# Performance work log

Measured on AMD Instinct MI355X. Metric: run time of the kernel, lower is better.

Reference implementation:

```python
import jax, jax.numpy as jnp
import numpy as np

MODES, WIDTH, DEPTH, IN_F, OUT_F, HID = 8, 16, 3, 1, 1, 64


def setup_inputs() -> dict:
    key = jax.random.key(0)
    ks = jax.random.split(key, 12)
    B, H, W = 8, 512, 512
    scale = 1.0 / (WIDTH * WIDTH)
    inp = {
        'x': jax.random.normal(ks[0], (B, IN_F, H, W), dtype=jnp.float32),
        'fc0_w': jax.random.normal(ks[1], (IN_F, WIDTH), dtype=jnp.float32) * 0.5,
        'fc0_b': jax.random.normal(ks[2], (WIDTH,), dtype=jnp.float32) * 0.1,
        # complex spectral weights stored as real/imag parts, stacked over depth
        'spec_wr': jax.random.normal(ks[3], (DEPTH, WIDTH, WIDTH, MODES, MODES), dtype=jnp.float32) * scale,
        'spec_wi': jax.random.normal(ks[4], (DEPTH, WIDTH, WIDTH, MODES, MODES), dtype=jnp.float32) * scale,
        # 1x1 convs as [depth, out, in] matmuls + bias
        'conv_w': jax.random.normal(ks[5], (DEPTH, WIDTH, WIDTH), dtype=jnp.float32) * 0.25,
        'conv_b': jax.random.normal(ks[6], (DEPTH, WIDTH), dtype=jnp.float32) * 0.1,
        'fc1_w': jax.random.normal(ks[7], (WIDTH, HID), dtype=jnp.float32) * 0.25,
        'fc1_b': jax.random.normal(ks[8], (HID,), dtype=jnp.float32) * 0.1,
        'fc2_w': jax.random.normal(ks[9], (HID, OUT_F), dtype=jnp.float32) * 0.125,
        'fc2_b': jax.random.normal(ks[10], (OUT_F,), dtype=jnp.float32) * 0.1,
    }
    return inp


def _spectral_conv(x, w):
    # x: [B, Ci, H, W] real; w: [Ci, Co, m, m] complex
    B, C, H, W = x.shape
    m = w.shape[2]
    x_ft = jnp.fft.rfft2(x, norm='forward')  # [B, Ci, H, W//2+1]
    out_modes = jnp.einsum('bixy,ioxy->boxy', x_ft[:, :, :m, :m], w)
    out_ft = jnp.zeros((B, w.shape[1], H, W // 2 + 1), dtype=out_modes.dtype)
    out_ft = out_ft.at[:, :, :m, :m].set(out_modes)
    return jnp.fft.irfft2(out_ft, s=(H, W), norm='forward')


def reference(x, fc0_w, fc0_b, spec_wr, spec_wi, conv_w, conv_b, fc1_w, fc1_b, fc2_w, fc2_b):
    # lift: [B,C,H,W] -> channels-last linear -> [B,width,H,W]
    h = jnp.einsum('bchw,cd->bdhw', x, fc0_w) + fc0_b[None, :, None, None]
    for d in range(DEPTH):
        w_c = (spec_wr[d] + 1j * spec_wi[d]).astype(jnp.complex64)
        y = _spectral_conv(h, w_c)
        local = jnp.einsum('bchw,oc->bohw', h, conv_w[d]) + conv_b[d][None, :, None, None]
        h = y + local
    h = jnp.einsum('bchw,cd->bdhw', h, fc1_w) + fc1_b[None, :, None, None]
    h = jax.nn.relu(h)
    out = jnp.einsum('bchw,cd->bdhw', h, fc2_w) + fc2_b[None, :, None, None]
    return out
```

## Files before the change

### kernel.cpp

```cpp
#include <hip/hip_runtime.h>
#include <math.h>

#define NB 8
#define NH 512
#define NW 512
#define ANG512 0.01227184630308513f
#define SPEC_D 16384

__device__ __forceinline__ void treduce16(float* p, float* tb, float* dst, int tid) {
    #pragma unroll
    for (int j = 0; j < 16; ++j) p[j] += __shfl_xor(p[j], 1);
    if (!(tid & 1)) {
        const int s = tid >> 1;
        #pragma unroll
        for (int j = 0; j < 16; ++j) tb[s * 17 + j] = p[j];
    }
    __syncthreads();
    {
        const int q = tid >> 4, g = tid & 15;
        float v = 0.f;
        #pragma unroll
        for (int j = 0; j < 8; ++j) v += tb[(g + 16 * j) * 17 + q];
        #pragma unroll
        for (int m = 1; m < 16; m <<= 1) v += __shfl_xor(v, m, 16);
        if (g == 0) dst[q] = v;
    }
    __syncthreads();
}

__global__ __launch_bounds__(256) void k_rowdft(const float* __restrict__ x,
                                                float* __restrict__ R) {
    __shared__ float tb[128 * 17];
    __shared__ float red[16];
    const int tid = threadIdx.x;
    const int b = blockIdx.x >> 9;
    const int row = blockIdx.x & 511;
    const float* xr = x + ((size_t)(b * NH + row)) * NW;
    const float xa = xr[tid], xb = xr[tid + 256];
    const float a = xa + xb, d = xa - xb;

    float p[16];
    float c1, s1;
    __sincosf(ANG512 * (float)tid, &s1, &c1);
    p[0] = a;      p[8] = 0.f;
    p[1] = d * c1; p[9] = -d * s1;
    {
        const float c2k = 2.f * c1;
        float ckm = 1.f, skm = 0.f, ck = c1, sk = s1;
        #pragma unroll
        for (int k = 2; k < 8; ++k) {
            const float cn = fmaf(c2k, ck, -ckm);
            const float sn = fmaf(c2k, sk, -skm);
            ckm = ck; skm = sk; ck = cn; sk = sn;
            const float v = (k & 1) ? d : a;
            p[k] = v * ck;
            p[8 + k] = -v * sk;
        }
    }
    treduce16(p, tb, red, tid);
    if (tid < 16) R[((size_t)(b * NH + row)) * 16 + tid] = red[tid];
}

__global__ __launch_bounds__(256) void k_modes(
        const float* __restrict__ R,
        const float* __restrict__ spec_wr, const float* __restrict__ spec_wi,
        const float* __restrict__ conv_w, const float* __restrict__ conv_b,
        const float* __restrict__ fc0_w, const float* __restrict__ fc0_b,
        const float* __restrict__ fc1_w, const float* __restrict__ fc1_b,
        float* __restrict__ AH, float* __restrict__ gvec, float* __restrict__ Kvec) {
    __shared__ float Wr_s[3][16][16][8];
    __shared__ float Wi_s[3][16][16][8];
    __shared__ float tb[128 * 17];
    __shared__ float X2[16];
    __shared__ float Xr[16][8], Xi[16][8];
    __shared__ float Fr[16][8], Fi[16][8];
    __shared__ float Ar[16][8], Ai[16][8];
    __shared__ float Pm[2][256];
    __shared__ float fc1_s[1024];
    __shared__ float ps[64];

    const int tid = threadIdx.x;
    const int bb = blockIdx.x >> 3;
    const int kx = blockIdx.x & 7;

    {
        const int i = tid >> 4, o = tid & 15;
        #pragma unroll
        for (int d = 0; d < 3; ++d) {
            const size_t base = (size_t)d * SPEC_D + ((size_t)(i * 16 + o) * 64 + kx * 8);
            const float4* pr = (const float4*)(spec_wr + base);
            const float4* pi = (const float4*)(spec_wi + base);
            *(float4*)(&Wr_s[d][i][o][0]) = pr[0];
            *(float4*)(&Wr_s[d][i][o][4]) = pr[1];
            *(float4*)(&Wi_s[d][i][o][0]) = pi[0];
            *(float4*)(&Wi_s[d][i][o][4]) = pi[1];
        }
    }
    {
        const int o = tid >> 4, c = tid & 15;
        float s = 0.f;
        for (int k = 0; k < 16; ++k)
            s += conv_w[512 + o * 16 + k] * conv_w[256 + k * 16 + c];
        Pm[0][tid] = s;
    }
    Pm[1][tid] = conv_w[512 + tid];
    #pragma unroll
    for (int k = 0; k < 4; ++k) fc1_s[tid + k * 256] = fc1_w[tid + k * 256];

    float p[16];
    #pragma unroll
    for (int j = 0; j < 16; ++j) p[j] = 0.f;
    #pragma unroll
    for (int r2 = 0; r2 < 2; ++r2) {
        const int row = tid + r2 * 256;
        const float4* rp4 = (const float4*)(R + ((size_t)(bb * NH + row)) * 16);
        const float4 q0 = rp4[0], q1 = rp4[1], q2 = rp4[2], q3 = rp4[3];
        const float re[8] = {q0.x, q0.y, q0.z, q0.w, q1.x, q1.y, q1.z, q1.w};
        const float im[8] = {q2.x, q2.y, q2.z, q2.w, q3.x, q3.y, q3.z, q3.w};
        const int m = (kx * row) & 511;
        float cm, sm;
        __sincosf(ANG512 * (float)m, &sm, &cm);
        #pragma unroll
        for (int k = 0; k < 8; ++k) {
            p[k]     += re[k] * cm + im[k] * sm;
            p[8 + k] += im[k] * cm - re[k] * sm;
        }
    }
    treduce16(p, tb, X2, tid);

    const bool act = (tid < 128);
    const int o = tid >> 3, ky = tid & 7;
    if (act) {
        const float inv = 1.f / (512.f * 512.f);
        float xr0 = fc0_w[o] * X2[ky] * inv;
        float xi0 = fc0_w[o] * X2[8 + ky] * inv;
        if (kx == 0 && ky == 0) xr0 += fc0_b[o];
        Xr[o][ky] = xr0; Xi[o][ky] = xi0;
        Ar[o][ky] = 0.f; Ai[o][ky] = 0.f;
    }
    __syncthreads();

    for (int dd = 0; dd < 3; ++dd) {
        if (act) {
            float fr = 0.f, fi = 0.f;
            #pragma unroll
            for (int i = 0; i < 16; ++i) {
                const float wre = Wr_s[dd][i][o][ky];
                const float wim = Wi_s[dd][i][o][ky];
                const float xr0 = Xr[i][ky], xi0 = Xi[i][ky];
                fr += xr0 * wre - xi0 * wim;
                fi += xr0 * wim + xi0 * wre;
            }
            Fr[o][ky] = fr; Fi[o][ky] = fi;
        }
        __syncthreads();
        float xnr = 0.f, xni = 0.f;
        if (act) {
            float ar, ai;
            if (dd == 2) {
                ar = Fr[o][ky]; ai = Fi[o][ky];
            } else {
                ar = 0.f; ai = 0.f;
                #pragma unroll
                for (int c = 0; c < 16; ++c) {
                    const float pv = Pm[dd][o * 16 + c];
                    ar = fmaf(pv, Fr[c][ky], ar);
                    ai = fmaf(pv, Fi[c][ky], ai);
                }
            }
            Ar[o][ky] += ar; Ai[o][ky] += ai;
            if (dd < 2) {
                const float fr0 = Fr[o][ky], fi0 = Fi[o][ky];
                if (ky == 0) {
                    if (kx == 0) { xnr = fr0; xni = 0.f; }
                    else         { xnr = 0.5f * fr0; xni = 0.5f * fi0; }
                } else { xnr = fr0; xni = fi0; }
                #pragma unroll
                for (int c = 0; c < 16; ++c) {
                    const float cc = conv_w[dd * 256 + o * 16 + c];
                    xnr = fmaf(cc, Xr[c][ky], xnr);
                    xni = fmaf(cc, Xi[c][ky], xni);
                }
                if (kx == 0 && ky == 0) xnr += conv_b[dd * 16 + o];
            }
        }
        __syncthreads();
        if (act && dd < 2) { Xr[o][ky] = xnr; Xi[o][ky] = xni; }
        __syncthreads();
    }

    #pragma unroll
    for (int k2 = 0; k2 < 2; ++k2) {
        const int idx = tid + k2 * 256;
        const int hd = idx >> 3, ky2 = idx & 7;
        float ar = 0.f, ai = 0.f;
        #pragma unroll
        for (int c = 0; c < 16; ++c) {
            const float f = fc1_s[c * 64 + hd];
            ar = fmaf(f, Ar[c][ky2], ar);
            ai = fmaf(f, Ai[c][ky2], ai);
        }
        const float ck = (ky2 == 0) ? 1.f : 2.f;
        const size_t off = ((((size_t)(bb * 64 + hd)) * 8 + ky2) * 8 + kx) * 2;
        AH[off] = ck * ar;
        AH[off + 1] = ck * ai;
    }

    if (blockIdx.x == 0) {
        if (tid < 16) {
            float su = 0.f, sb = 0.f;
            for (int c = 0; c < 16; ++c) {
                su += conv_w[tid * 16 + c] * fc0_w[c];
                sb += conv_w[tid * 16 + c] * fc0_b[c];
            }
            ps[tid] = su; ps[16 + tid] = sb;
        }
        __syncthreads();
        if (tid < 16) {
            float dv = 0.f, ev = conv_b[32 + tid];
            for (int k = 0; k < 16; ++k) {
                dv += Pm[0][tid * 16 + k] * ps[k];
                ev += Pm[0][tid * 16 + k] * (ps[16 + k] + conv_b[k]);
                ev += conv_w[512 + tid * 16 + k] * conv_b[16 + k];
            }
            ps[32 + tid] = dv; ps[48 + tid] = ev;
        }
        __syncthreads();
        if (tid < 64) {
            float g = 0.f, K = fc1_b[tid];
            for (int c = 0; c < 16; ++c) {
                g = fmaf(fc1_w[c * 64 + tid], ps[32 + c], g);
                K = fmaf(fc1_w[c * 64 + tid], ps[48 + c], K);
            }
            gvec[tid] = g; Kvec[tid] = K;
        }
    }
}

__global__ __launch_bounds__(256, 2) void k_head(
        const float* __restrict__ x, const float* __restrict__ AH,
        const float* __restrict__ gvec, const float* __restrict__ Kvec,
        const float* __restrict__ fc2_w, const float* __restrict__ fc2_b,
        float* __restrict__ out) {
    __shared__ float WHr[4][512];
    __shared__ float WHi[4][512];

    const int tid = threadIdx.x;
    const int b = blockIdx.x >> 7;
    const int rp = blockIdx.x & 127;
    const int rl = tid >> 6;
    const int row = rp * 4 + rl;
    const int w0 = tid & 63;

    const float* xp = x + ((size_t)(b * NH + row)) * NW + w0;
    float xv[8];
    #pragma unroll
    for (int j = 0; j < 8; ++j) xv[j] = xp[j * 64];

    {
        float c1, s1;
        __sincosf(ANG512 * (float)row, &s1, &c1);
        float ctr[8], str[8];
        ctr[0] = 1.f; str[0] = 0.f; ctr[1] = c1; str[1] = s1;
        const float c2k = 2.f * c1;
        #pragma unroll
        for (int k = 2; k < 8; ++k) {
            ctr[k] = fmaf(c2k, ctr[k - 1], -ctr[k - 2]);
            str[k] = fmaf(c2k, str[k - 1], -str[k - 2]);
        }
        #pragma unroll
        for (int j = 0; j < 8; ++j) {
            const int idx = w0 + j * 64;
            const int hd = idx >> 3, ky = idx & 7;
            const float4* ap = (const float4*)(AH + ((size_t)(b * 64 + hd) * 8 + ky) * 16);
            const float4 a0 = ap[0], a1 = ap[1], a2 = ap[2], a3 = ap[3];
            float wr = a0.x, wi = a0.y;
            wr = fmaf(a0.z, ctr[1], wr); wr = fmaf(-a0.w, str[1], wr);
            wi = fmaf(a0.z, str[1], wi); wi = fmaf(a0.w, ctr[1], wi);
            wr = fmaf(a1.x, ctr[2], wr); wr = fmaf(-a1.y, str[2], wr);
            wi = fmaf(a1.x, str[2], wi); wi = fmaf(a1.y, ctr[2], wi);
            wr = fmaf(a1.z, ctr[3], wr); wr = fmaf(-a1.w, str[3], wr);
            wi = fmaf(a1.z, str[3], wi); wi = fmaf(a1.w, ctr[3], wi);
            wr = fmaf(a2.x, ctr[4], wr); wr = fmaf(-a2.y, str[4], wr);
            wi = fmaf(a2.x, str[4], wi); wi = fmaf(a2.y, ctr[4], wi);
            wr = fmaf(a2.z, ctr[5], wr); wr = fmaf(-a2.w, str[5], wr);
            wi = fmaf(a2.z, str[5], wi); wi = fmaf(a2.w, ctr[5], wi);
            wr = fmaf(a3.x, ctr[6], wr); wr = fmaf(-a3.y, str[6], wr);
            wi = fmaf(a3.x, str[6], wi); wi = fmaf(a3.y, ctr[6], wi);
            wr = fmaf(a3.z, ctr[7], wr); wr = fmaf(-a3.w, str[7], wr);
            wi = fmaf(a3.z, str[7], wi); wi = fmaf(a3.w, ctr[7], wi);
            if (ky == 0) wr += Kvec[hd];
            WHr[rl][idx] = wr;
            WHi[rl][idx] = wi;
        }
    }
    __syncthreads();

    {
        float c1, s1;
        __sincosf(ANG512 * (float)w0, &s1, &c1);
        float ct[8], st[8];
        ct[0] = 1.f; st[0] = 0.f; ct[1] = c1; st[1] = s1;
        const float c2k = 2.f * c1;
        #pragma unroll
        for (int k = 2; k < 8; ++k) {
            ct[k] = fmaf(c2k, ct[k - 1], -ct[k - 2]);
            st[k] = fmaf(c2k, st[k - 1], -st[k - 2]);
        }
        const float r2c = 0.70710678118654752f;
        const float* WR = &WHr[rl][0];
        const float* WI = &WHi[rl][0];
        const float fc2b = fc2_b[0];
        float acc[8];
        #pragma unroll
        for (int j = 0; j < 8; ++j) acc[j] = fc2b;

        #pragma unroll 4
        for (int hd = 0; hd < 64; ++hd) {
            const float4* r4 = (const float4*)(WR + hd * 8);
            const float4 wa = r4[0], wb = r4[1];
            const float4* i4 = (const float4*)(WI + hd * 8);
            const float4 va = i4[0], vb = i4[1];
            const float tr0 = wa.x;
            const float tr1 = wa.y * ct[1] - va.y * st[1];
            const float ti1 = wa.y * st[1] + va.y * ct[1];
            const float tr2 = wa.z * ct[2] - va.z * st[2];
            const float ti2 = wa.z * st[2] + va.z * ct[2];
            const float tr3 = wa.w * ct[3] - va.w * st[3];
            const float ti3 = wa.w * st[3] + va.w * ct[3];
            const float tr4 = wb.x * ct[4] - vb.x * st[4];
            const float tr5 = wb.y * ct[5] - vb.y * st[5];
            const float ti5 = wb.y * st[5] + vb.y * ct[5];
            const float tr6 = wb.z * ct[6] - vb.z * st[6];
            const float ti6 = wb.z * st[6] + vb.z * ct[6];
            const float tr7 = wb.w * ct[7] - vb.w * st[7];
            const float ti7 = wb.w * st[7] + vb.w * ct[7];

            const float gh = gvec[hd];
            const float w2 = fc2_w[hd];

            const float A0 = tr0 + tr4, A2 = tr2 + tr6;
            const float E = A0 + A2, D = A0 - A2;
            const float B13 = (tr1 + tr5) + (tr3 + tr7);
            const float U = (ti1 + ti5) - (ti3 + ti7);
            const float s0 = fmaf(gh, xv[0], E + B13);
            const float s2 = fmaf(gh, xv[2], D - U);
            const float s4 = fmaf(gh, xv[4], E - B13);
            const float s6 = fmaf(gh, xv[6], D + U);
            acc[0] = fmaf(fmaxf(s0, 0.f), w2, acc[0]);
            acc[2] = fmaf(fmaxf(s2, 0.f), w2, acc[2]);
            acc[4] = fmaf(fmaxf(s4, 0.f), w2, acc[4]);
            acc[6] = fmaf(fmaxf(s6, 0.f), w2, acc[6]);

            const float P = tr0 - tr4, Q = ti6 - ti2;
            const float E2 = P + Q, D2 = P - Q;
            const float B2 = r2c * (((tr1 - ti1) - (tr5 - ti5)) + ((tr7 + ti7) - (tr3 + ti3)));
            const float U2 = r2c * (((tr1 + ti1) - (tr5 + ti5)) - ((tr3 - ti3) + (ti7 - tr7)));
            const float s1p = fmaf(gh, xv[1], E2 + B2);
            const float s3p = fmaf(gh, xv[3], D2 - U2);
            const float s5p = fmaf(gh, xv[5], E2 - B2);
            const float s7p = fmaf(gh, xv[7], D2 + U2);
            acc[1] = fmaf(fmaxf(s1p, 0.f), w2, acc[1]);
            acc[3] = fmaf(fmaxf(s3p, 0.f), w2, acc[3]);
            acc[5] = fmaf(fmaxf(s5p, 0.f), w2, acc[5]);
            acc[7] = fmaf(fmaxf(s7p, 0.f), w2, acc[7]);
        }
        float* op = out + ((size_t)(b * NH + row)) * NW + w0;
        #pragma unroll
        for (int j = 0; j < 8; ++j) op[j * 64] = acc[j];
    }
}

extern "C" void kernel_launch(void* const* d_in, const int* in_sizes, int n_in,
                              void* d_out, int out_size, void* d_ws, size_t ws_size,
                              hipStream_t stream) {
    const float* x       = (const float*)d_in[0];
    const float* fc0_w   = (const float*)d_in[1];
    const float* fc0_b   = (const float*)d_in[2];
    const float* spec_wr = (const float*)d_in[3];
    const float* spec_wi = (const float*)d_in[4];
    const float* conv_w  = (const float*)d_in[5];
    const float* conv_b  = (const float*)d_in[6];
    const float* fc1_w   = (const float*)d_in[7];
    const float* fc1_b   = (const float*)d_in[8];
    const float* fc2_w   = (const float*)d_in[9];
    const float* fc2_b   = (const float*)d_in[10];
    float* outp = (float*)d_out;

    char* ws = (char*)d_ws;
    float* R  = (float*)ws;
    float* AH = (float*)(ws + 262144);
    float* gv = (float*)(ws + 524288);
    float* Kv = (float*)(ws + 524288 + 256);

    k_rowdft<<<NB * NH, 256, 0, stream>>>(x, R);
    k_modes<<<NB * 8, 256, 0, stream>>>(R, spec_wr, spec_wi, conv_w, conv_b,
                                        fc0_w, fc0_b, fc1_w, fc1_b, AH, gv, Kv);
    k_head<<<NB * 128, 256, 0, stream>>>(x, AH, gv, Kv, fc2_w, fc2_b, outp);
}
```

Measured before the change: 144.9 us.

## Fuse three kernels into one persistent kernel with grid-wide atomic barriers

Merges the row-DFT, mode-mixing and head kernels into one 1024-block kernel separated by two software grid barriers built on agent-scope atomics, with a memset to reset the counters. This removes two kernel launches and their inter-kernel gaps, and it relies on all 1024 blocks being co-resident, which the launch bound of 4 blocks per CU and a shared-memory union are meant to allow. The mode stage now reads spectral weights directly from global memory instead of staging them in shared memory. If the blocks cannot all be resident at once the barrier deadlocks, and the mode phase runs on only 64 blocks while the rest wait.

```diff
diff --git a/kernel.cpp b/kernel.cpp
--- a/kernel.cpp
+++ b/kernel.cpp
@@ -6,6 +6,21 @@
 #define NW 512
 #define ANG512 0.01227184630308513f
 #define SPEC_D 16384
+#define NBLK 1024
+
+#define TB   0
+#define RED  2176
+#define XR   2192
+#define XI   2320
+#define FR   2448
+#define FI   2576
+#define AR   2704
+#define AI   2832
+#define PM   2960
+#define FC1  3472
+#define WHR  0
+#define WHI  2048
+#define SMEMF 4496
 
 __device__ __forceinline__ void treduce16(float* p, float* tb, float* dst, int tid) {
     #pragma unroll
@@ -28,226 +43,220 @@
     __syncthreads();
 }
 
-__global__ __launch_bounds__(256) void k_rowdft(const float* __restrict__ x,
-                                                float* __restrict__ R) {
-    __shared__ float tb[128 * 17];
-    __shared__ float red[16];
-    const int tid = threadIdx.x;
-    const int b = blockIdx.x >> 9;
-    const int row = blockIdx.x & 511;
-    const float* xr = x + ((size_t)(b * NH + row)) * NW;
-    const float xa = xr[tid], xb = xr[tid + 256];
-    const float a = xa + xb, d = xa - xb;
-
-    float p[16];
-    float c1, s1;
-    __sincosf(ANG512 * (float)tid, &s1, &c1);
-    p[0] = a;      p[8] = 0.f;
-    p[1] = d * c1; p[9] = -d * s1;
-    {
-        const float c2k = 2.f * c1;
-        float ckm = 1.f, skm = 0.f, ck = c1, sk = s1;
-        #pragma unroll
-        for (int k = 2; k < 8; ++k) {
-            const float cn = fmaf(c2k, ck, -ckm);
-            const float sn = fmaf(c2k, sk, -skm);
-            ckm = ck; skm = sk; ck = cn; sk = sn;
-            const float v = (k & 1) ? d : a;
-            p[k] = v * ck;
-            p[8 + k] = -v * sk;
-        }
-    }
-    treduce16(p, tb, red, tid);
-    if (tid < 16) R[((size_t)(b * NH + row)) * 16 + tid] = red[tid];
+__device__ __forceinline__ void gridbar(int* bar, int idx, int tid) {
+    __syncthreads();
+    if (tid == 0) {
+        __hip_atomic_fetch_add(bar + idx, 1, __ATOMIC_ACQ_REL, __HIP_MEMORY_SCOPE_AGENT);
+        while (__hip_atomic_load(bar + idx, __ATOMIC_ACQUIRE, __HIP_MEMORY_SCOPE_AGENT) < NBLK) {
+            __builtin_amdgcn_s_sleep(8);
+        }
+    }
+    __syncthreads();
 }
 
-__global__ __launch_bounds__(256) void k_modes(
-        const float* __restrict__ R,
-        const float* __restrict__ spec_wr, const float* __restrict__ spec_wi,
-        const float* __restrict__ conv_w, const float* __restrict__ conv_b,
-        const float* __restrict__ fc0_w, const float* __restrict__ fc0_b,
-        const float* __restrict__ fc1_w, const float* __restrict__ fc1_b,
-        float* __restrict__ AH, float* __restrict__ gvec, float* __restrict__ Kvec) {
-    __shared__ float Wr_s[3][16][16][8];
-    __shared__ float Wi_s[3][16][16][8];
-    __shared__ float tb[128 * 17];
-    __shared__ float X2[16];
-    __shared__ float Xr[16][8], Xi[16][8];
-    __shared__ float Fr[16][8], Fi[16][8];
-    __shared__ float Ar[16][8], Ai[16][8];
-    __shared__ float Pm[2][256];
-    __shared__ float fc1_s[1024];
-    __shared__ float ps[64];
-
-    const int tid = threadIdx.x;
-    const int bb = blockIdx.x >> 3;
-    const int kx = blockIdx.x & 7;
-
-    {
-        const int i = tid >> 4, o = tid & 15;
-        #pragma unroll
-        for (int d = 0; d < 3; ++d) {
-            const size_t base = (size_t)d * SPEC_D + ((size_t)(i * 16 + o) * 64 + kx * 8);
-            const float4* pr = (const float4*)(spec_wr + base);
-            const float4* pi = (const float4*)(spec_wi + base);
-            *(float4*)(&Wr_s[d][i][o][0]) = pr[0];
-            *(float4*)(&Wr_s[d][i][o][4]) = pr[1];
-            *(float4*)(&Wi_s[d][i][o][0]) = pi[0];
-            *(float4*)(&Wi_s[d][i][o][4]) = pi[1];
-        }
-    }
-    {
-        const int o = tid >> 4, c = tid & 15;
-        float s = 0.f;
-        for (int k = 0; k < 16; ++k)
-            s += conv_w[512 + o * 16 + k] * conv_w[256 + k * 16 + c];
-        Pm[0][tid] = s;
-    }
-    Pm[1][tid] = conv_w[512 + tid];
-    #pragma unroll
-    for (int k = 0; k < 4; ++k) fc1_s[tid + k * 256] = fc1_w[tid + k * 256];
-
-    float p[16];
-    #pragma unroll
-    for (int j = 0; j < 16; ++j) p[j] = 0.f;
-    #pragma unroll
-    for (int r2 = 0; r2 < 2; ++r2) {
-        const int row = tid + r2 * 256;
-        const float4* rp4 = (const float4*)(R + ((size_t)(bb * NH + row)) * 16);
-        const float4 q0 = rp4[0], q1 = rp4[1], q2 = rp4[2], q3 = rp4[3];
-        const float re[8] = {q0.x, q0.y, q0.z, q0.w, q1.x, q1.y, q1.z, q1.w};
-        const float im[8] = {q2.x, q2.y, q2.z, q2.w, q3.x, q3.y, q3.z, q3.w};
-        const int m = (kx * row) & 511;
-        float cm, sm;
-        __sincosf(ANG512 * (float)m, &sm, &cm);
-        #pragma unroll
-        for (int k = 0; k < 8; ++k) {
-            p[k]     += re[k] * cm + im[k] * sm;
-            p[8 + k] += im[k] * cm - re[k] * sm;
-        }
-    }
-    treduce16(p, tb, X2, tid);
-
-    const bool act = (tid < 128);
-    const int o = tid >> 3, ky = tid & 7;
-    if (act) {
-        const float inv = 1.f / (512.f * 512.f);
-        float xr0 = fc0_w[o] * X2[ky] * inv;
-        float xi0 = fc0_w[o] * X2[8 + ky] * inv;
-        if (kx == 0 && ky == 0) xr0 += fc0_b[o];
-        Xr[o][ky] = xr0; Xi[o][ky] = xi0;
-        Ar[o][ky] = 0.f; Ai[o][ky] = 0.f;
-    }
-    __syncthreads();
-
-    for (int dd = 0; dd < 3; ++dd) {
-        if (act) {
-            float fr = 0.f, fi = 0.f;
-            #pragma unroll
-            for (int i = 0; i < 16; ++i) {
-                const float wre = Wr_s[dd][i][o][ky];
-                const float wim = Wi_s[dd][i][o][ky];
-                const float xr0 = Xr[i][ky], xi0 = Xi[i][ky];
-                fr += xr0 * wre - xi0 * wim;
-                fi += xr0 * wim + xi0 * wre;
-            }
-            Fr[o][ky] = fr; Fi[o][ky] = fi;
-        }
-        __syncthreads();
-        float xnr = 0.f, xni = 0.f;
-        if (act) {
-            float ar, ai;
-            if (dd == 2) {
-                ar = Fr[o][ky]; ai = Fi[o][ky];
-            } else {
-                ar = 0.f; ai = 0.f;
-                #pragma unroll
-                for (int c = 0; c < 16; ++c) {
-                    const float pv = Pm[dd][o * 16 + c];
-                    ar = fmaf(pv, Fr[c][ky], ar);
-                    ai = fmaf(pv, Fi[c][ky], ai);
-                }
-            }
-            Ar[o][ky] += ar; Ai[o][ky] += ai;
-            if (dd < 2) {
-                const float fr0 = Fr[o][ky], fi0 = Fi[o][ky];
-                if (ky == 0) {
-                    if (kx == 0) { xnr = fr0; xni = 0.f; }
-                    else         { xnr = 0.5f * fr0; xni = 0.5f * fi0; }
-                } else { xnr = fr0; xni = fi0; }
-                #pragma unroll
-                for (int c = 0; c < 16; ++c) {
-                    const float cc = conv_w[dd * 256 + o * 16 + c];
-                    xnr = fmaf(cc, Xr[c][ky], xnr);
-                    xni = fmaf(cc, Xi[c][ky], xni);
-                }
-                if (kx == 0 && ky == 0) xnr += conv_b[dd * 16 + o];
-            }
-        }
-        __syncthreads();
-        if (act && dd < 2) { Xr[o][ky] = xnr; Xi[o][ky] = xni; }
-        __syncthreads();
-    }
-
-    #pragma unroll
-    for (int k2 = 0; k2 < 2; ++k2) {
-        const int idx = tid + k2 * 256;
-        const int hd = idx >> 3, ky2 = idx & 7;
-        float ar = 0.f, ai = 0.f;
-        #pragma unroll
-        for (int c = 0; c < 16; ++c) {
-            const float f = fc1_s[c * 64 + hd];
-            ar = fmaf(f, Ar[c][ky2], ar);
-            ai = fmaf(f, Ai[c][ky2], ai);
-        }
-        const float ck = (ky2 == 0) ? 1.f : 2.f;
-        const size_t off = ((((size_t)(bb * 64 + hd)) * 8 + ky2) * 8 + kx) * 2;
-        AH[off] = ck * ar;
-        AH[off + 1] = ck * ai;
-    }
-
-    if (blockIdx.x == 0) {
-        if (tid < 16) {
-            float su = 0.f, sb = 0.f;
-            for (int c = 0; c < 16; ++c) {
-                su += conv_w[tid * 16 + c] * fc0_w[c];
-                sb += conv_w[tid * 16 + c] * fc0_b[c];
-            }
-            ps[tid] = su; ps[16 + tid] = sb;
-        }
-        __syncthreads();
-        if (tid < 16) {
-            float dv = 0.f, ev = conv_b[32 + tid];
-            for (int k = 0; k < 16; ++k) {
-                dv += Pm[0][tid * 16 + k] * ps[k];
-                ev += Pm[0][tid * 16 + k] * (ps[16 + k] + conv_b[k]);
-                ev += conv_w[512 + tid * 16 + k] * conv_b[16 + k];
-            }
-            ps[32 + tid] = dv; ps[48 + tid] = ev;
-        }
-        __syncthreads();
-        if (tid < 64) {
-            float g = 0.f, K = fc1_b[tid];
-            for (int c = 0; c < 16; ++c) {
-                g = fmaf(fc1_w[c * 64 + tid], ps[32 + c], g);
-                K = fmaf(fc1_w[c * 64 + tid], ps[48 + c], K);
-            }
-            gvec[tid] = g; Kvec[tid] = K;
-        }
-    }
-}
-
-__global__ __launch_bounds__(256, 2) void k_head(
-        const float* __restrict__ x, const float* __restrict__ AH,
-        const float* __restrict__ gvec, const float* __restrict__ Kvec,
-        const float* __restrict__ fc2_w, const float* __restrict__ fc2_b,
-        float* __restrict__ out) {
-    __shared__ float WHr[4][512];
-    __shared__ float WHi[4][512];
-
+__global__ __launch_bounds__(256, 4) void k_fused(
+    const float* __restrict__ x,
+    const float* __restrict__ spec_wr, const float* __restrict__ spec_wi,
+    const float* __restrict__ conv_w, const float* __restrict__ conv_b,
+    const float* __restrict__ fc0_w, const float* __restrict__ fc0_b,
+    const float* __restrict__ fc1_w, const float* __restrict__ fc1_b,
+    const float* __restrict__ fc2_w, const float* __restrict__ fc2_b,
+    float* __restrict__ out,
+    float* __restrict__ R, float* __restrict__ AH,
+    float* __restrict__ gvec, float* __restrict__ Kvec, int* bar)
+{
+    __shared__ float smem[SMEMF];
     const int tid = threadIdx.x;
     const int b = blockIdx.x >> 7;
     const int rp = blockIdx.x & 127;
+
+    for (int ri = 0; ri < 4; ++ri) {
+        const int row = rp * 4 + ri;
+        const float* xr = x + ((size_t)(b * NH + row)) * NW;
+        const float xa = xr[tid], xb = xr[tid + 256];
+        const float a = xa + xb, d = xa - xb;
+        float p[16];
+        float c1, s1;
+        __sincosf(ANG512 * (float)tid, &s1, &c1);
+        p[0] = a;      p[8] = 0.f;
+        p[1] = d * c1; p[9] = -d * s1;
+        {
+            const float c2k = 2.f * c1;
+            float ckm = 1.f, skm = 0.f, ck = c1, sk = s1;
+            #pragma unroll
+            for (int k = 2; k < 8; ++k) {
+                const float cn = fmaf(c2k, ck, -ckm);
+                const float sn = fmaf(c2k, sk, -skm);
+                ckm = ck; skm = sk; ck = cn; sk = sn;
+                const float v = (k & 1) ? d : a;
+                p[k] = v * ck;
+                p[8 + k] = -v * sk;
+            }
+        }
+        treduce16(p, smem + TB, smem + RED, tid);
+        if (tid < 16) R[((size_t)(b * NH + row)) * 16 + tid] = smem[RED + tid];
+        __syncthreads();
+    }
+
+    gridbar(bar, 0, tid);
+
+    if (blockIdx.x < 64) {
+        const int bb = blockIdx.x >> 3;
+        const int kx = blockIdx.x & 7;
+
+        {
+            const int o = tid >> 4, c = tid & 15;
+            float s = 0.f;
+            for (int k = 0; k < 16; ++k)
+                s += conv_w[512 + o * 16 + k] * conv_w[256 + k * 16 + c];
+            smem[PM + tid] = s;
+            smem[PM + 256 + tid] = conv_w[512 + tid];
+        }
+        #pragma unroll
+        for (int k = 0; k < 4; ++k) smem[FC1 + tid + k * 256] = fc1_w[tid + k * 256];
+
+        float p[16];
+        #pragma unroll
+        for (int j = 0; j < 16; ++j) p[j] = 0.f;
+        #pragma unroll
+        for (int r2 = 0; r2 < 2; ++r2) {
+            const int row = tid + r2 * 256;
+            const float4* rp4 = (const float4*)(R + ((size_t)(bb * NH + row)) * 16);
+            const float4 q0 = rp4[0], q1 = rp4[1], q2 = rp4[2], q3 = rp4[3];
+            const float re[8] = {q0.x, q0.y, q0.z, q0.w, q1.x, q1.y, q1.z, q1.w};
+            const float im[8] = {q2.x, q2.y, q2.z, q2.w, q3.x, q3.y, q3.z, q3.w};
+            const int m = (kx * row) & 511;
+            float cm, sm;
+            __sincosf(ANG512 * (float)m, &sm, &cm);
+            #pragma unroll
+            for (int k = 0; k < 8; ++k) {
+                p[k]     += re[k] * cm + im[k] * sm;
+                p[8 + k] += im[k] * cm - re[k] * sm;
+            }
+        }
+        treduce16(p, smem + TB, smem + RED, tid);
+
+        const bool act = (tid < 128);
+        const int o = tid >> 3, ky = tid & 7;
+        if (act) {
+            const float inv = 1.f / (512.f * 512.f);
+            float xr0 = fc0_w[o] * smem[RED + ky] * inv;
+            float xi0 = fc0_w[o] * smem[RED + 8 + ky] * inv;
+            if (kx == 0 && ky == 0) xr0 += fc0_b[o];
+            smem[XR + o * 8 + ky] = xr0;
+            smem[XI + o * 8 + ky] = xi0;
+            smem[AR + o * 8 + ky] = 0.f;
+            smem[AI + o * 8 + ky] = 0.f;
+        }
+        __syncthreads();
+
+        for (int dd = 0; dd < 3; ++dd) {
+            if (act) {
+                const float* wrp = spec_wr + (size_t)dd * SPEC_D + (size_t)o * 64 + kx * 8 + ky;
+                const float* wip = spec_wi + (size_t)dd * SPEC_D + (size_t)o * 64 + kx * 8 + ky;
+                float fr = 0.f, fi = 0.f;
+                #pragma unroll
+                for (int i = 0; i < 16; ++i) {
+                    const float wre = wrp[(size_t)i * 1024];
+                    const float wim = wip[(size_t)i * 1024];
+                    const float xr0 = smem[XR + i * 8 + ky], xi0 = smem[XI + i * 8 + ky];
+                    fr += xr0 * wre - xi0 * wim;
+                    fi += xr0 * wim + xi0 * wre;
+                }
+                smem[FR + o * 8 + ky] = fr;
+                smem[FI + o * 8 + ky] = fi;
+            }
+            __syncthreads();
+            float xnr = 0.f, xni = 0.f;
+            if (act) {
+                float ar, ai;
+                if (dd == 2) {
+                    ar = smem[FR + o * 8 + ky]; ai = smem[FI + o * 8 + ky];
+                } else {
+                    ar = 0.f; ai = 0.f;
+                    #pragma unroll
+                    for (int c = 0; c < 16; ++c) {
+                        const float pv = smem[PM + dd * 256 + o * 16 + c];
+                        ar = fmaf(pv, smem[FR + c * 8 + ky], ar);
+                        ai = fmaf(pv, smem[FI + c * 8 + ky], ai);
+                    }
+                }
+                smem[AR + o * 8 + ky] += ar;
+                smem[AI + o * 8 + ky] += ai;
+                if (dd < 2) {
+                    const float fr0 = smem[FR + o * 8 + ky], fi0 = smem[FI + o * 8 + ky];
+                    if (ky == 0) {
+                        if (kx == 0) { xnr = fr0; xni = 0.f; }
+                        else         { xnr = 0.5f * fr0; xni = 0.5f * fi0; }
+                    } else { xnr = fr0; xni = fi0; }
+                    #pragma unroll
+                    for (int c = 0; c < 16; ++c) {
+                        const float cc = conv_w[dd * 256 + o * 16 + c];
+                        xnr = fmaf(cc, smem[XR + c * 8 + ky], xnr);
+                        xni = fmaf(cc, smem[XI + c * 8 + ky], xni);
+                    }
+                    if (kx == 0 && ky == 0) xnr += conv_b[dd * 16 + o];
+                }
+            }
+            __syncthreads();
+            if (act && dd < 2) {
+                smem[XR + o * 8 + ky] = xnr;
+                smem[XI + o * 8 + ky] = xni;
+            }
+            __syncthreads();
+        }
+
+        #pragma unroll
+        for (int k2 = 0; k2 < 2; ++k2) {
+            const int idx = tid + k2 * 256;
+            const int hd = idx >> 3, ky2 = idx & 7;
+            float ar = 0.f, ai = 0.f;
+            #pragma unroll
+            for (int c = 0; c < 16; ++c) {
+                const float f = smem[FC1 + c * 64 + hd];
+                ar = fmaf(f, smem[AR + c * 8 + ky2], ar);
+                ai = fmaf(f, smem[AI + c * 8 + ky2], ai);
+            }
+            const float ck = (ky2 == 0) ? 1.f : 2.f;
+            const size_t off = ((((size_t)(bb * 64 + hd)) * 8 + ky2) * 8 + kx) * 2;
+            AH[off] = ck * ar;
+            AH[off + 1] = ck * ai;
+        }
+
+        if (blockIdx.x == 0) {
+            __syncthreads();
+            if (tid < 16) {
+                float su = 0.f, sb = 0.f;
+                for (int c = 0; c < 16; ++c) {
+                    su += conv_w[tid * 16 + c] * fc0_w[c];
+                    sb += conv_w[tid * 16 + c] * fc0_b[c];
+                }
+                smem[TB + tid] = su; smem[TB + 16 + tid] = sb;
+            }
+            __syncthreads();
+            if (tid < 16) {
+                float dv = 0.f, ev = conv_b[32 + tid];
+                for (int k = 0; k < 16; ++k) {
+                    dv += smem[PM + tid * 16 + k] * smem[TB + k];
+                    ev += smem[PM + tid * 16 + k] * (smem[TB + 16 + k] + conv_b[k]);
+                    ev += conv_w[512 + tid * 16 + k] * conv_b[16 + k];
+                }
+                smem[TB + 32 + tid] = dv; smem[TB + 48 + tid] = ev;
+            }
+            __syncthreads();
+            if (tid < 64) {
+                float g = 0.f, K = fc1_b[tid];
+                for (int c = 0; c < 16; ++c) {
+                    g = fmaf(fc1_w[c * 64 + tid], smem[TB + 32 + c], g);
+                    K = fmaf(fc1_w[c * 64 + tid], smem[TB + 48 + c], K);
+                }
+                gvec[tid] = g; Kvec[tid] = K;
+            }
+        }
+    }
+
+    gridbar(bar, 1, tid);
+
     const int rl = tid >> 6;
     const int row = rp * 4 + rl;
     const int w0 = tid & 63;
@@ -288,10 +297,10 @@
             wr = fmaf(a3.x, ctr[6], wr); wr = fmaf(-a3.y, str[6], wr);
             wi = fmaf(a3.x, str[6], wi); wi = fmaf(a3.y, ctr[6], wi);
             wr = fmaf(a3.z, ctr[7], wr); wr = fmaf(-a3.w, str[7], wr);
-            wi = fmaf(a3.z, str[7], wi); wi = fmaf(a3.w, ctr[7], wi);
+            wi = fmaf(a3.w, ctr[7], wi); wi = fmaf(a3.z, str[7], wi);
             if (ky == 0) wr += Kvec[hd];
-            WHr[rl][idx] = wr;
-            WHi[rl][idx] = wi;
+            smem[WHR + rl * 512 + idx] = wr;
+            smem[WHI + rl * 512 + idx] = wi;
         }
     }
     __syncthreads();
@@ -308,8 +317,8 @@
             st[k] = fmaf(c2k, st[k - 1], -st[k - 2]);
         }
         const float r2c = 0.70710678118654752f;
-        const float* WR = &WHr[rl][0];
-        const float* WI = &WHi[rl][0];
+        const float* WR = smem + WHR + rl * 512;
+        const float* WI = smem + WHI + rl * 512;
         const float fc2b = fc2_b[0];
         float acc[8];
         #pragma unroll
@@ -388,13 +397,14 @@
     float* outp = (float*)d_out;
 
     char* ws = (char*)d_ws;
-    float* R  = (float*)ws;
-    float* AH = (float*)(ws + 262144);
-    float* gv = (float*)(ws + 524288);
-    float* Kv = (float*)(ws + 524288 + 256);
-
-    k_rowdft<<<NB * NH, 256, 0, stream>>>(x, R);
-    k_modes<<<NB * 8, 256, 0, stream>>>(R, spec_wr, spec_wi, conv_w, conv_b,
-                                        fc0_w, fc0_b, fc1_w, fc1_b, AH, gv, Kv);
-    k_head<<<NB * 128, 256, 0, stream>>>(x, AH, gv, Kv, fc2_w, fc2_b, outp);
+    float* R   = (float*)ws;
+    float* AH  = (float*)(ws + 262144);
+    float* gv  = (float*)(ws + 524288);
+    float* Kv  = (float*)(ws + 524288 + 256);
+    int*   bar = (int*)(ws + 524288 + 512);
+
+    hipMemsetAsync(bar, 0, 2 * sizeof(int), stream);
+    k_fused<<<NBLK, 256, 0, stream>>>(x, spec_wr, spec_wi, conv_w, conv_b,
+                                      fc0_w, fc0_b, fc1_w, fc1_b, fc2_w, fc2_b,
+                                      outp, R, AH, gv, Kv, bar);
 }
```

Measured after the change: 364.0 us. +151.3%, slower.
